# Optimization experiments

Hardware: AMD Instinct MI355X
Metric: run time of the kernel (lower is better)

Reference implementation:

```python
import jax, jax.numpy as jnp
import numpy as np

N_NODES = 100000
N_EDGES = 1600000
IN_DIM, HID_DIM, OUT_DIM = 2, 64, 1


def setup_inputs() -> dict:
    key = jax.random.key(0)
    ks = jax.random.split(key, 8)
    x = jax.random.normal(ks[0], (N_NODES, IN_DIM), dtype=jnp.float32)
    edge_index = jax.random.randint(ks[1], (2, N_EDGES), 0, N_NODES, dtype=jnp.int64)
    # GCNConv weights (glorot-ish scale) and biases
    def lin(k, fan_in, fan_out):
        s = 1.0 / np.sqrt(fan_in)
        return jax.random.uniform(k, (fan_in, fan_out), jnp.float32, -s, s)
    return {
        "x": x,
        "edge_index": edge_index,
        "W1": lin(ks[2], IN_DIM, HID_DIM), "b1": jnp.zeros((HID_DIM,), jnp.float32),
        "W2": lin(ks[3], HID_DIM, HID_DIM), "b2": jnp.zeros((HID_DIM,), jnp.float32),
        "W3": lin(ks[4], HID_DIM, OUT_DIM), "b3": jnp.zeros((OUT_DIM,), jnp.float32),
    }


def _gcn_norm(edge_index, n_nodes):
    # add self-loops, symmetric normalization: norm_e = deg[src]^-1/2 * deg[dst]^-1/2
    loops = jnp.arange(n_nodes, dtype=edge_index.dtype)
    src = jnp.concatenate([edge_index[0], loops])
    dst = jnp.concatenate([edge_index[1], loops])
    deg = jax.ops.segment_sum(jnp.ones_like(src, dtype=jnp.float32), dst,
                              num_segments=n_nodes)
    dinv = jnp.where(deg > 0, jax.lax.rsqrt(jnp.maximum(deg, 1.0)), 0.0)
    norm = dinv[src] * dinv[dst]  # [E+N]
    return src, dst, norm


def _gcn_layer(h, src, dst, norm, W, b, n_nodes):
    h = h @ W                     # [N, d_out] (transform-then-propagate)
    msg = h[src] * norm[:, None]  # gather + scale: [E+N, d_out]
    out = jax.ops.segment_sum(msg, dst, num_segments=n_nodes)  # scatter-add
    return out + b


def reference(x, edge_index, W1, b1, W2, b2, W3, b3):
    n = x.shape[0]
    src, dst, norm = _gcn_norm(edge_index, n)
    h = jax.nn.relu(_gcn_layer(x, src, dst, norm, W1, b1, n))
    h = jax.nn.relu(_gcn_layer(h, src, dst, norm, W2, b2, n))
    return _gcn_layer(h, src, dst, norm, W3, b3, n)  # [N, 1]
```

## Files before the change

kernel.cpp:

```cpp
#include <hip/hip_runtime.h>
#include <hip/hip_fp16.h>

#define THREADS 256
#define BKT_SHIFT 9
#define BKT_NODES 512
#define BKT_CAP 12288
#define RPW 8

typedef _Float16 h2 __attribute__((ext_vector_type(2)));

__device__ inline h2 u2h(unsigned u) { union { unsigned u; h2 h; } c; c.u = u; return c.h; }
__device__ inline unsigned h2u(h2 h) { union { unsigned u; h2 h; } c; c.h = h; return c.u; }
__device__ inline float fdot2f(h2 a, h2 b, float c) { return __builtin_amdgcn_fdot2(a, b, c, false); }

__global__ void k_binA(const int* __restrict__ src, const int* __restrict__ dst,
                       int* __restrict__ bucket_cnt, unsigned int* __restrict__ binned,
                       int E, int NB) {
    __shared__ int hist[256];
    __shared__ int cur[256];
    int t = threadIdx.x;
    if (t < NB) hist[t] = 0;
    __syncthreads();
    int chunk = (E + gridDim.x - 1) / gridDim.x;
    int e0 = blockIdx.x * chunk;
    int e1 = min(E, e0 + chunk);
    for (int e = e0 + t; e < e1; e += THREADS) atomicAdd(&hist[dst[e] >> BKT_SHIFT], 1);
    __syncthreads();
    if (t < NB) {
        int c = hist[t];
        cur[t] = c ? atomicAdd(&bucket_cnt[t], c) : 0;
    }
    __syncthreads();
    for (int e = e0 + t; e < e1; e += THREADS) {
        int d = dst[e];
        int b = d >> BKT_SHIFT;
        int pos = atomicAdd(&cur[b], 1);
        if (pos < BKT_CAP)
            binned[(size_t)b * BKT_CAP + pos] =
                (unsigned int)src[e] | ((unsigned int)(d & (BKT_NODES - 1)) << 17);
    }
}

__global__ void k_scanB(const int* __restrict__ bucket_cnt, int* __restrict__ bucket_base,
                        int* __restrict__ row_ptr, int NB, int N, int E) {
    __shared__ int sh[1024];
    int t = threadIdx.x;
    int v = (t < NB) ? bucket_cnt[t] : 0;
    sh[t] = v;
    __syncthreads();
    for (int off = 1; off < 1024; off <<= 1) {
        int u = (t >= off) ? sh[t - off] : 0;
        __syncthreads();
        sh[t] += u;
        __syncthreads();
    }
    if (t < NB) bucket_base[t] = sh[t] - v;
    if (t == 0) row_ptr[N] = E;
}

__global__ void k_binB(const unsigned int* __restrict__ binned, const int* __restrict__ bucket_cnt,
                       const int* __restrict__ bucket_base, const float2* __restrict__ x,
                       int* __restrict__ row_ptr, float* __restrict__ dinv,
                       float2* __restrict__ xs, int* __restrict__ esrc, int N) {
    __shared__ int h[BKT_NODES], sc[BKT_NODES], cur[BKT_NODES];
    int b = blockIdx.x, t = threadIdx.x;
    int cntb = min(bucket_cnt[b], BKT_CAP);
    int base = bucket_base[b];
    h[t] = 0;
    __syncthreads();
    const unsigned int* bp = binned + (size_t)b * BKT_CAP;
    for (int e = t; e < cntb; e += BKT_NODES) atomicAdd(&h[bp[e] >> 17], 1);
    __syncthreads();
    sc[t] = h[t];
    __syncthreads();
    for (int off = 1; off < BKT_NODES; off <<= 1) {
        int u = (t >= off) ? sc[t - off] : 0;
        __syncthreads();
        sc[t] += u;
        __syncthreads();
    }
    int node = b * BKT_NODES + t;
    if (node < N) {
        int excl = sc[t] - h[t];
        row_ptr[node] = base + excl;
        cur[t] = excl;
        float dv = rsqrtf((float)(h[t] + 1));
        dinv[node] = dv;
        float2 v = x[node];
        xs[node] = make_float2(v.x * dv, v.y * dv);
    }
    __syncthreads();
    for (int e = t; e < cntb; e += BKT_NODES) {
        unsigned int p = bp[e];
        int pos = atomicAdd(&cur[p >> 17], 1);
        esrc[base + pos] = (int)(p & 0x1FFFFu);
    }
}

__global__ void k_g2l12(const int* __restrict__ row_ptr, const int* __restrict__ esrc,
                        const float* __restrict__ dinv, const float2* __restrict__ xs,
                        const float* __restrict__ W1, const float* __restrict__ b1,
                        const float* __restrict__ W2, __half* __restrict__ A, int n) {
    int tid = threadIdx.x;
    int j = tid & 63;
    int gw = blockIdx.x * (THREADS / 64) + (tid >> 6);
    int row0 = gw * RPW;
    if (row0 >= n) return;

    h2 w2p[32];
#pragma unroll
    for (int m = 0; m < 32; ++m) {
        h2 w;
        w[0] = (_Float16)W2[(2 * m) * 64 + j];
        w[1] = (_Float16)W2[(2 * m + 1) * 64 + j];
        w2p[m] = w;
    }
    int jj = (j < 32) ? j : 0;
    float w1xa = W1[2 * jj],     w1ya = W1[64 + 2 * jj],     b1a = b1[2 * jj];
    float w1xb = W1[2 * jj + 1], w1yb = W1[64 + 2 * jj + 1], b1b = b1[2 * jj + 1];

    int rend = min(n, row0 + RPW);
    for (int row = row0; row < rend; ++row) {
        int e0 = row_ptr[row], e1 = row_ptr[row + 1];
        float ax = 0.0f, ay = 0.0f;
        for (int e = e0 + j; e < e1; e += 64) {
            float2 v = xs[esrc[e]];
            ax += v.x;
            ay += v.y;
        }
#pragma unroll
        for (int m = 1; m < 64; m <<= 1) {
            ax += __shfl_xor(ax, m, 64);
            ay += __shfl_xor(ay, m, 64);
        }
        float2 own = xs[row];
        float dv = dinv[row];
        float gx = (ax + own.x) * dv;
        float gy = (ay + own.y) * dv;
        float ha = fmaxf(gx * w1xa + gy * w1ya + b1a, 0.0f);
        float hb = fmaxf(gx * w1xb + gy * w1yb + b1b, 0.0f);
        h2 hpk;
        hpk[0] = (_Float16)ha;
        hpk[1] = (_Float16)hb;
        unsigned hpu = h2u(hpk);
        float a0 = 0.0f, a1 = 0.0f, a2 = 0.0f, a3 = 0.0f;
#pragma unroll
        for (int m = 0; m < 32; m += 4) {
            unsigned p0 = (unsigned)__builtin_amdgcn_readlane((int)hpu, m);
            unsigned p1 = (unsigned)__builtin_amdgcn_readlane((int)hpu, m + 1);
            unsigned p2 = (unsigned)__builtin_amdgcn_readlane((int)hpu, m + 2);
            unsigned p3 = (unsigned)__builtin_amdgcn_readlane((int)hpu, m + 3);
            a0 = fdot2f(u2h(p0), w2p[m], a0);
            a1 = fdot2f(u2h(p1), w2p[m + 1], a1);
            a2 = fdot2f(u2h(p2), w2p[m + 2], a2);
            a3 = fdot2f(u2h(p3), w2p[m + 3], a3);
        }
        float rA = ((a0 + a1) + (a2 + a3)) * dv;
        float rB = __shfl_xor(rA, 1, 64);
        if ((j & 1) == 0) {
            __half2 hv = __floats2half2_rn(rA, rB);
            *(__half2*)&A[(size_t)row * 64 + j] = hv;
        }
    }
}

__device__ inline void add8d(float a[8], uint4 u, h2 c10, h2 c01) {
    h2 p0 = u2h(u.x), p1 = u2h(u.y), p2 = u2h(u.z), p3 = u2h(u.w);
    a[0] = fdot2f(p0, c10, a[0]); a[1] = fdot2f(p0, c01, a[1]);
    a[2] = fdot2f(p1, c10, a[2]); a[3] = fdot2f(p1, c01, a[3]);
    a[4] = fdot2f(p2, c10, a[4]); a[5] = fdot2f(p2, c01, a[5]);
    a[6] = fdot2f(p3, c10, a[6]); a[7] = fdot2f(p3, c01, a[7]);
}

__global__ void k_gather64f(const int* __restrict__ row_ptr, const int* __restrict__ esrc,
                            const float* __restrict__ dinv, const __half* __restrict__ tt,
                            const float* __restrict__ b2, const float* __restrict__ W3,
                            float* __restrict__ tt3, int n) {
    int tid = blockIdx.x * blockDim.x + threadIdx.x;
    int i = tid >> 6;
    if (i >= n) return;
    int lane = tid & 63;
    int q = lane >> 3;
    int c = lane & 7;
    h2 c10, c01;
    c10[0] = (_Float16)1.0f; c10[1] = (_Float16)0.0f;
    c01[0] = (_Float16)0.0f; c01[1] = (_Float16)1.0f;
    float a[8];
#pragma unroll
    for (int d = 0; d < 8; ++d) a[d] = 0.0f;
    if (q == 0) add8d(a, *(const uint4*)&tt[(size_t)i * 64 + c * 8], c10, c01);
    int e0 = row_ptr[i], e1 = row_ptr[i + 1];
    int e = e0 + q;
    for (; e + 8 < e1; e += 16) {
        int s0 = esrc[e], s1 = esrc[e + 8];
        uint4 u0 = *(const uint4*)&tt[(size_t)s0 * 64 + c * 8];
        uint4 u1 = *(const uint4*)&tt[(size_t)s1 * 64 + c * 8];
        add8d(a, u0, c10, c01);
        add8d(a, u1, c10, c01);
    }
    if (e < e1) add8d(a, *(const uint4*)&tt[(size_t)esrc[e] * 64 + c * 8], c10, c01);
#pragma unroll
    for (int m = 8; m <= 32; m <<= 1) {
#pragma unroll
        for (int d = 0; d < 8; ++d) a[d] += __shfl_xor(a[d], m, 64);
    }
    if (q == 0) {
        float dv = dinv[i];
        const float4 blo = *(const float4*)&b2[c * 8];
        const float4 bhi = *(const float4*)&b2[c * 8 + 4];
        const float4 wlo = *(const float4*)&W3[c * 8];
        const float4 whi = *(const float4*)&W3[c * 8 + 4];
        float p = fmaxf(a[0] * dv + blo.x, 0.0f) * wlo.x
                + fmaxf(a[1] * dv + blo.y, 0.0f) * wlo.y
                + fmaxf(a[2] * dv + blo.z, 0.0f) * wlo.z
                + fmaxf(a[3] * dv + blo.w, 0.0f) * wlo.w
                + fmaxf(a[4] * dv + bhi.x, 0.0f) * whi.x
                + fmaxf(a[5] * dv + bhi.y, 0.0f) * whi.y
                + fmaxf(a[6] * dv + bhi.z, 0.0f) * whi.z
                + fmaxf(a[7] * dv + bhi.w, 0.0f) * whi.w;
#pragma unroll
        for (int m = 1; m < 8; m <<= 1) p += __shfl_xor(p, m, 64);
        if (c == 0) tt3[i] = p * dv;
    }
}

__global__ void k_gather1(const int* __restrict__ row_ptr, const int* __restrict__ esrc,
                          const float* __restrict__ dinv, const float* __restrict__ tt3,
                          const float* __restrict__ b3, float* __restrict__ out, int n) {
    int i = blockIdx.x * blockDim.x + threadIdx.x;
    if (i >= n) return;
    float acc = tt3[i];
    int e = row_ptr[i], e1 = row_ptr[i + 1];
    for (; e + 4 <= e1; e += 4) {
        acc += tt3[esrc[e]] + tt3[esrc[e + 1]] + tt3[esrc[e + 2]] + tt3[esrc[e + 3]];
    }
    for (; e < e1; ++e) acc += tt3[esrc[e]];
    out[i] = acc * dinv[i] + b3[0];
}

extern "C" void kernel_launch(void* const* d_in, const int* in_sizes, int n_in,
                              void* d_out, int out_size, void* d_ws, size_t ws_size,
                              hipStream_t stream) {
    const float* x  = (const float*)d_in[0];
    const int*   ei = (const int*)d_in[1];
    const float* W1 = (const float*)d_in[2];
    const float* b1 = (const float*)d_in[3];
    const float* W2 = (const float*)d_in[4];
    const float* b2 = (const float*)d_in[5];
    const float* W3 = (const float*)d_in[6];
    const float* b3 = (const float*)d_in[7];
    float* out = (float*)d_out;

    const int N = in_sizes[0] / 2;
    const int E = in_sizes[1] / 2;
    const int* src = ei;
    const int* dst = ei + E;
    const int NB = (N + BKT_NODES - 1) >> BKT_SHIFT;

    char* ws = (char*)d_ws;
    float* dinv = (float*)ws;
    size_t off = ((size_t)N * sizeof(float) + 255) & ~(size_t)255;
    float* Af = (float*)(ws + off);
    __half* A = (__half*)Af;
    float* tt3 = Af + (size_t)N * 64;
    float2* xs = (float2*)(tt3 + N);
    int* bucket_cnt = (int*)(xs + N);
    int* bucket_base = bucket_cnt + 256;
    int* row_ptr = bucket_base + 256;
    int* esrc = row_ptr + N + 2;
    unsigned int* binned = (unsigned int*)Af;

    dim3 blk(THREADS);
    dim3 gN((N + THREADS - 1) / THREADS);
    dim3 gN64((int)(((long long)N * 64 + THREADS - 1) / THREADS));

    hipMemsetAsync(bucket_cnt, 0, 256 * sizeof(int), stream);
    k_binA<<<dim3(512), blk, 0, stream>>>(src, dst, bucket_cnt, binned, E, NB);
    k_scanB<<<dim3(1), dim3(1024), 0, stream>>>(bucket_cnt, bucket_base, row_ptr, NB, N, E);
    k_binB<<<dim3(NB), dim3(BKT_NODES), 0, stream>>>(binned, bucket_cnt, bucket_base,
                                                     (const float2*)x, row_ptr, dinv, xs, esrc, N);

    {
        int waves = (N + RPW - 1) / RPW;
        int blocks = (waves + (THREADS / 64) - 1) / (THREADS / 64);
        k_g2l12<<<dim3(blocks), blk, 0, stream>>>(row_ptr, esrc, dinv, xs, W1, b1, W2, A, N);
    }

    k_gather64f<<<gN64, blk, 0, stream>>>(row_ptr, esrc, dinv, A, b2, W3, tt3, N);

    k_gather1<<<gN, blk, 0, stream>>>(row_ptr, esrc, dinv, tt3, b3, out, N);
}
```

Before: 150.5 us.

## Store pre-shifted byte offsets in esrc and narrow gather64 to 8-byte lanes

The CSR build now stores each source index multiplied by 128, the byte stride of a half-precision 64-wide row, so the 64-dim gather adds the offset directly without index multiply or 64-bit address math. The other kernels shift the offset back down. The 64-dim gather now uses 16 lanes per edge with 8-byte loads and 4 edges per lane group instead of 8 lanes with 16-byte loads, unrolled 4-way. This gives more independent loads in flight per row, at the cost of smaller load width and more loop iterations. Offsets are kept in 32 bits, which assumes N*128 fits in 32 bits.

```diff
diff --git a/kernel.cpp b/kernel.cpp
--- a/kernel.cpp
+++ b/kernel.cpp
@@ -93,7 +93,7 @@
     for (int e = t; e < cntb; e += BKT_NODES) {
         unsigned int p = bp[e];
         int pos = atomicAdd(&cur[p >> 17], 1);
-        esrc[base + pos] = (int)(p & 0x1FFFFu);
+        esrc[base + pos] = (int)((p & 0x1FFFFu) << 7);
     }
 }
 
@@ -124,7 +124,7 @@
         int e0 = row_ptr[row], e1 = row_ptr[row + 1];
         float ax = 0.0f, ay = 0.0f;
         for (int e = e0 + j; e < e1; e += 64) {
-            float2 v = xs[esrc[e]];
+            float2 v = xs[(unsigned)esrc[e] >> 7];
             ax += v.x;
             ay += v.y;
         }
@@ -164,12 +164,10 @@
     }
 }
 
-__device__ inline void add8d(float a[8], uint4 u, h2 c10, h2 c01) {
-    h2 p0 = u2h(u.x), p1 = u2h(u.y), p2 = u2h(u.z), p3 = u2h(u.w);
+__device__ inline void add4d(float a[4], uint2 u, h2 c10, h2 c01) {
+    h2 p0 = u2h(u.x), p1 = u2h(u.y);
     a[0] = fdot2f(p0, c10, a[0]); a[1] = fdot2f(p0, c01, a[1]);
     a[2] = fdot2f(p1, c10, a[2]); a[3] = fdot2f(p1, c01, a[3]);
-    a[4] = fdot2f(p2, c10, a[4]); a[5] = fdot2f(p2, c01, a[5]);
-    a[6] = fdot2f(p3, c10, a[6]); a[7] = fdot2f(p3, c01, a[7]);
 }
 
 __global__ void k_gather64f(const int* __restrict__ row_ptr, const int* __restrict__ esrc,
@@ -180,46 +178,49 @@
     int i = tid >> 6;
     if (i >= n) return;
     int lane = tid & 63;
-    int q = lane >> 3;
-    int c = lane & 7;
+    int q = lane >> 4;
+    int c = lane & 15;
     h2 c10, c01;
     c10[0] = (_Float16)1.0f; c10[1] = (_Float16)0.0f;
     c01[0] = (_Float16)0.0f; c01[1] = (_Float16)1.0f;
-    float a[8];
-#pragma unroll
-    for (int d = 0; d < 8; ++d) a[d] = 0.0f;
-    if (q == 0) add8d(a, *(const uint4*)&tt[(size_t)i * 64 + c * 8], c10, c01);
+    const char* ttb = (const char*)tt + c * 8;
+    float a[4];
+#pragma unroll
+    for (int d = 0; d < 4; ++d) a[d] = 0.0f;
+    if (q == 0) add4d(a, *(const uint2*)(ttb + (size_t)i * 128), c10, c01);
     int e0 = row_ptr[i], e1 = row_ptr[i + 1];
     int e = e0 + q;
-    for (; e + 8 < e1; e += 16) {
-        int s0 = esrc[e], s1 = esrc[e + 8];
-        uint4 u0 = *(const uint4*)&tt[(size_t)s0 * 64 + c * 8];
-        uint4 u1 = *(const uint4*)&tt[(size_t)s1 * 64 + c * 8];
-        add8d(a, u0, c10, c01);
-        add8d(a, u1, c10, c01);
-    }
-    if (e < e1) add8d(a, *(const uint4*)&tt[(size_t)esrc[e] * 64 + c * 8], c10, c01);
-#pragma unroll
-    for (int m = 8; m <= 32; m <<= 1) {
-#pragma unroll
-        for (int d = 0; d < 8; ++d) a[d] += __shfl_xor(a[d], m, 64);
+    for (; e + 12 < e1; e += 16) {
+        unsigned o0 = (unsigned)esrc[e],     o1 = (unsigned)esrc[e + 4];
+        unsigned o2 = (unsigned)esrc[e + 8], o3 = (unsigned)esrc[e + 12];
+        uint2 u0 = *(const uint2*)(ttb + o0);
+        uint2 u1 = *(const uint2*)(ttb + o1);
+        uint2 u2 = *(const uint2*)(ttb + o2);
+        uint2 u3 = *(const uint2*)(ttb + o3);
+        add4d(a, u0, c10, c01);
+        add4d(a, u1, c10, c01);
+        add4d(a, u2, c10, c01);
+        add4d(a, u3, c10, c01);
+    }
+    for (; e < e1; e += 4) {
+        uint2 u = *(const uint2*)(ttb + (unsigned)esrc[e]);
+        add4d(a, u, c10, c01);
+    }
+#pragma unroll
+    for (int m = 16; m <= 32; m <<= 1) {
+#pragma unroll
+        for (int d = 0; d < 4; ++d) a[d] += __shfl_xor(a[d], m, 64);
     }
     if (q == 0) {
         float dv = dinv[i];
-        const float4 blo = *(const float4*)&b2[c * 8];
-        const float4 bhi = *(const float4*)&b2[c * 8 + 4];
-        const float4 wlo = *(const float4*)&W3[c * 8];
-        const float4 whi = *(const float4*)&W3[c * 8 + 4];
-        float p = fmaxf(a[0] * dv + blo.x, 0.0f) * wlo.x
-                + fmaxf(a[1] * dv + blo.y, 0.0f) * wlo.y
-                + fmaxf(a[2] * dv + blo.z, 0.0f) * wlo.z
-                + fmaxf(a[3] * dv + blo.w, 0.0f) * wlo.w
-                + fmaxf(a[4] * dv + bhi.x, 0.0f) * whi.x
-                + fmaxf(a[5] * dv + bhi.y, 0.0f) * whi.y
-                + fmaxf(a[6] * dv + bhi.z, 0.0f) * whi.z
-                + fmaxf(a[7] * dv + bhi.w, 0.0f) * whi.w;
-#pragma unroll
-        for (int m = 1; m < 8; m <<= 1) p += __shfl_xor(p, m, 64);
+        const float4 b = *(const float4*)&b2[c * 4];
+        const float4 w = *(const float4*)&W3[c * 4];
+        float p = fmaxf(a[0] * dv + b.x, 0.0f) * w.x
+                + fmaxf(a[1] * dv + b.y, 0.0f) * w.y
+                + fmaxf(a[2] * dv + b.z, 0.0f) * w.z
+                + fmaxf(a[3] * dv + b.w, 0.0f) * w.w;
+#pragma unroll
+        for (int m = 1; m < 16; m <<= 1) p += __shfl_xor(p, m, 64);
         if (c == 0) tt3[i] = p * dv;
     }
 }
@@ -232,9 +233,10 @@
     float acc = tt3[i];
     int e = row_ptr[i], e1 = row_ptr[i + 1];
     for (; e + 4 <= e1; e += 4) {
-        acc += tt3[esrc[e]] + tt3[esrc[e + 1]] + tt3[esrc[e + 2]] + tt3[esrc[e + 3]];
-    }
-    for (; e < e1; ++e) acc += tt3[esrc[e]];
+        acc += tt3[(unsigned)esrc[e] >> 7] + tt3[(unsigned)esrc[e + 1] >> 7]
+             + tt3[(unsigned)esrc[e + 2] >> 7] + tt3[(unsigned)esrc[e + 3] >> 7];
+    }
+    for (; e < e1; ++e) acc += tt3[(unsigned)esrc[e] >> 7];
     out[i] = acc * dinv[i] + b3[0];
 }
 
```

Result: slower. 155.2 us (+3.1%).

## Use 16 lanes per node in 64-wide gather and store pre-scaled byte offsets

Applied to the files above, without the earlier changes.

The 64-dim gather kernel now assigns 16 lanes per destination node instead of 64, each processing two edge streams with four loads in flight, and drops the cross-group shuffle reduction to one step. Edge source indices are stored pre-shifted by 7 so they serve directly as byte offsets into the 128-byte fp16 rows, and the other consumers shift them back. This reduces idle lanes for low-degree nodes (average degree about 16) and removes reduction shuffles and address arithmetic. It packs the node index into 24 bits, which still covers the 100k nodes.

```diff
diff --git a/kernel.cpp b/kernel.cpp
--- a/kernel.cpp
+++ b/kernel.cpp
@@ -93,7 +93,7 @@
     for (int e = t; e < cntb; e += BKT_NODES) {
         unsigned int p = bp[e];
         int pos = atomicAdd(&cur[p >> 17], 1);
-        esrc[base + pos] = (int)(p & 0x1FFFFu);
+        esrc[base + pos] = (int)((p & 0x1FFFFu) << 7);
     }
 }
 
@@ -124,7 +124,7 @@
         int e0 = row_ptr[row], e1 = row_ptr[row + 1];
         float ax = 0.0f, ay = 0.0f;
         for (int e = e0 + j; e < e1; e += 64) {
-            float2 v = xs[esrc[e]];
+            float2 v = xs[(unsigned)esrc[e] >> 7];
             ax += v.x;
             ay += v.y;
         }
@@ -177,33 +177,39 @@
                             const float* __restrict__ b2, const float* __restrict__ W3,
                             float* __restrict__ tt3, int n) {
     int tid = blockIdx.x * blockDim.x + threadIdx.x;
-    int i = tid >> 6;
+    int i = tid >> 4;
     if (i >= n) return;
-    int lane = tid & 63;
+    int lane = tid & 15;
     int q = lane >> 3;
     int c = lane & 7;
     h2 c10, c01;
     c10[0] = (_Float16)1.0f; c10[1] = (_Float16)0.0f;
     c01[0] = (_Float16)0.0f; c01[1] = (_Float16)1.0f;
+    const char* ttb = (const char*)tt + c * 16;
     float a[8];
 #pragma unroll
     for (int d = 0; d < 8; ++d) a[d] = 0.0f;
-    if (q == 0) add8d(a, *(const uint4*)&tt[(size_t)i * 64 + c * 8], c10, c01);
+    if (q == 0) add8d(a, *(const uint4*)(ttb + (size_t)i * 128), c10, c01);
     int e0 = row_ptr[i], e1 = row_ptr[i + 1];
     int e = e0 + q;
-    for (; e + 8 < e1; e += 16) {
-        int s0 = esrc[e], s1 = esrc[e + 8];
-        uint4 u0 = *(const uint4*)&tt[(size_t)s0 * 64 + c * 8];
-        uint4 u1 = *(const uint4*)&tt[(size_t)s1 * 64 + c * 8];
+    for (; e + 6 < e1; e += 8) {
+        unsigned o0 = (unsigned)esrc[e],     o1 = (unsigned)esrc[e + 2];
+        unsigned o2 = (unsigned)esrc[e + 4], o3 = (unsigned)esrc[e + 6];
+        uint4 u0 = *(const uint4*)(ttb + o0);
+        uint4 u1 = *(const uint4*)(ttb + o1);
+        uint4 u2 = *(const uint4*)(ttb + o2);
+        uint4 u3 = *(const uint4*)(ttb + o3);
         add8d(a, u0, c10, c01);
         add8d(a, u1, c10, c01);
-    }
-    if (e < e1) add8d(a, *(const uint4*)&tt[(size_t)esrc[e] * 64 + c * 8], c10, c01);
-#pragma unroll
-    for (int m = 8; m <= 32; m <<= 1) {
-#pragma unroll
-        for (int d = 0; d < 8; ++d) a[d] += __shfl_xor(a[d], m, 64);
-    }
+        add8d(a, u2, c10, c01);
+        add8d(a, u3, c10, c01);
+    }
+    for (; e < e1; e += 2) {
+        uint4 u = *(const uint4*)(ttb + (unsigned)esrc[e]);
+        add8d(a, u, c10, c01);
+    }
+#pragma unroll
+    for (int d = 0; d < 8; ++d) a[d] += __shfl_xor(a[d], 8, 64);
     if (q == 0) {
         float dv = dinv[i];
         const float4 blo = *(const float4*)&b2[c * 8];
@@ -218,8 +224,9 @@
                 + fmaxf(a[5] * dv + bhi.y, 0.0f) * whi.y
                 + fmaxf(a[6] * dv + bhi.z, 0.0f) * whi.z
                 + fmaxf(a[7] * dv + bhi.w, 0.0f) * whi.w;
-#pragma unroll
-        for (int m = 1; m < 8; m <<= 1) p += __shfl_xor(p, m, 64);
+        p += __shfl_xor(p, 1, 64);
+        p += __shfl_xor(p, 2, 64);
+        p += __shfl_xor(p, 4, 64);
         if (c == 0) tt3[i] = p * dv;
     }
 }
@@ -232,9 +239,10 @@
     float acc = tt3[i];
     int e = row_ptr[i], e1 = row_ptr[i + 1];
     for (; e + 4 <= e1; e += 4) {
-        acc += tt3[esrc[e]] + tt3[esrc[e + 1]] + tt3[esrc[e + 2]] + tt3[esrc[e + 3]];
-    }
-    for (; e < e1; ++e) acc += tt3[esrc[e]];
+        acc += tt3[(unsigned)esrc[e] >> 7] + tt3[(unsigned)esrc[e + 1] >> 7]
+             + tt3[(unsigned)esrc[e + 2] >> 7] + tt3[(unsigned)esrc[e + 3] >> 7];
+    }
+    for (; e < e1; ++e) acc += tt3[(unsigned)esrc[e] >> 7];
     out[i] = acc * dinv[i] + b3[0];
 }
 
@@ -272,7 +280,7 @@
 
     dim3 blk(THREADS);
     dim3 gN((N + THREADS - 1) / THREADS);
-    dim3 gN64((int)(((long long)N * 64 + THREADS - 1) / THREADS));
+    dim3 gN16((int)(((long long)N * 16 + THREADS - 1) / THREADS));
 
     hipMemsetAsync(bucket_cnt, 0, 256 * sizeof(int), stream);
     k_binA<<<dim3(512), blk, 0, stream>>>(src, dst, bucket_cnt, binned, E, NB);
@@ -286,7 +294,7 @@
         k_g2l12<<<dim3(blocks), blk, 0, stream>>>(row_ptr, esrc, dinv, xs, W1, b1, W2, A, N);
     }
 
-    k_gather64f<<<gN64, blk, 0, stream>>>(row_ptr, esrc, dinv, A, b2, W3, tt3, N);
+    k_gather64f<<<gN16, blk, 0, stream>>>(row_ptr, esrc, dinv, A, b2, W3, tt3, N);
 
     k_gather1<<<gN, blk, 0, stream>>>(row_ptr, esrc, dinv, tt3, b3, out, N);
 }
```

Measured after the change: 135.2 us. -10.2%, faster.
